# Performance work log

Measured on AMD Instinct MI355X. Metric: run time of the kernel, lower is better.

The kernel has to match this reference:

```python
import jax, jax.numpy as jnp
import numpy as np

BOX = 100.0      # points live in [0, BOX)^3
STRIDE = 128     # > BOX/voxel_size, used for linearizing 3D voxel coords


def setup_inputs() -> dict:
    key = jax.random.key(0)
    k1, k2 = jax.random.split(key)
    N, C = 2_000_000, 32
    positions = jax.random.uniform(k1, (N, 3), dtype=jnp.float32) * BOX
    features = jax.random.normal(k2, (N, C), dtype=jnp.float32)
    voxel_size = jnp.ones((), dtype=jnp.float32)
    return {"positions": positions, "features": features, "voxel_size": voxel_size}


def reference(positions, features, voxel_size):
    """VoxelPooling(position_fn='center', feature_fn='max').

    Output is padded to N rows (M <= N real voxels); `valid` marks real voxels.
    Voxel grid is aligned to the origin; pooled position is the voxel center.
    """
    N = positions.shape[0]
    # integer voxel coordinates (positions are non-negative here)
    coords = jnp.floor(positions / voxel_size).astype(jnp.int32)           # [N,3]
    lin = coords[:, 0] + STRIDE * coords[:, 1] + STRIDE * STRIDE * coords[:, 2]  # [N]
    # compact unique voxels; jit-compatible with fixed size=N, pad with -1
    uniq, inv = jnp.unique(lin, size=N, fill_value=-1, return_inverse=True)
    # per-voxel max over features (empty segments get dtype-min, masked below)
    pooled_features = jax.ops.segment_max(features, inv, num_segments=N)   # [N,C]
    # decode voxel coords from linear key -> voxel centers
    cz = uniq // (STRIDE * STRIDE)
    rem = uniq % (STRIDE * STRIDE)
    cy = rem // STRIDE
    cx = rem % STRIDE
    centers = (jnp.stack([cx, cy, cz], axis=-1).astype(positions.dtype) + 0.5) * voxel_size
    valid = uniq >= 0                                                      # [N]
    pooled_positions = jnp.where(valid[:, None], centers, 0.0)
    pooled_features = jnp.where(valid[:, None], pooled_features, 0.0)
    return pooled_positions, pooled_features, valid
```

## Files before the change

### kernel.cpp

```cpp
#include <hip/hip_runtime.h>
#include <stdint.h>

#define STRIDE 128
#define NVOX (STRIDE * STRIDE * STRIDE)
#define BINVOX 512
#define NBIN (NVOX / BINVOX)
#define HB 256
#define HT 1024
#define NSEG 16
#define SEGBINS (NBIN / NSEG)
#define CAP 1536
#define LINCAP 8192

typedef unsigned long long u64;
typedef float nfloat4 __attribute__((ext_vector_type(4)));

__device__ __forceinline__ uint32_t enc_f32(float f) {
  uint32_t u = __float_as_uint(f);
  return (u & 0x80000000u) ? ~u : (u | 0x80000000u);
}
__device__ __forceinline__ float dec_f32(uint32_t e) {
  uint32_t u = (e & 0x80000000u) ? (e & 0x7fffffffu) : ~e;
  return __uint_as_float(u);
}

__device__ __forceinline__ uint32_t cnt_eq1(uint32_t w) {
  uint32_t y = w ^ 0x01010101u;
  uint32_t z = ~(((y & 0x7F7F7F7Fu) + 0x7F7F7F7Fu) | y | 0x7F7F7F7Fu);
  return __popc(z);
}

__device__ __forceinline__ uint32_t src_of(uint32_t u, const uint32_t* csum,
                                           const uint32_t* offs) {
  uint32_t lo = 0, hi = HB - 1;
  #pragma unroll
  for (int it = 0; it < 8; ++it) {
    uint32_t mid = (lo + hi) >> 1;
    bool gt = csum[mid] > u;
    hi = gt ? mid : hi;
    lo = gt ? lo : mid + 1;
  }
  uint32_t prev = lo ? csum[lo - 1] : 0u;
  return offs[lo] + (u - prev);
}

__device__ __forceinline__ void nt_zero4(void* p) {
  nfloat4 z = {0.f, 0.f, 0.f, 0.f};
  __builtin_nontemporal_store(z, (nfloat4*)p);
}

__global__ __launch_bounds__(HT) void k_build(
    const float* __restrict__ pos, const float* __restrict__ vs_p,
    uint8_t* __restrict__ bytemap, uint32_t* __restrict__ loff,
    uint32_t* __restrict__ pairs, uint32_t* __restrict__ sync,
    float* __restrict__ out_pos, float* __restrict__ out_feat,
    float* __restrict__ out_valid, int n, int vbound, int srow) {
  __shared__ uint32_t h[NBIN];
  __shared__ uint32_t wsum[HT / 64];
  __shared__ uint32_t linbuf[LINCAP];
  int t = threadIdx.x;

  if (blockIdx.x >= HB) {
    size_t gid = (size_t)(blockIdx.x - HB) * HT + t;
    int row = vbound + (int)(gid >> 3);
    int q = (int)(gid & 7);
    if (row >= n) return;
    if (row < srow)
      nt_zero4(((float4*)out_feat) + (size_t)row * 8 + q);
    if (q == 0) {
      out_pos[(size_t)row * 3 + 0] = 0.f;
      out_pos[(size_t)row * 3 + 1] = 0.f;
      out_pos[(size_t)row * 3 + 2] = 0.f;
      out_valid[row] = 0.f;
    }
    return;
  }

  int b = blockIdx.x;
  if (b == 0 && t == 0) *sync = 0u;
  for (int k = t; k < NBIN; k += HT) h[k] = 0u;
  __syncthreads();
  int chunk = (n + HB - 1) / HB;
  int i0 = b * chunk, i1 = min(n, i0 + chunk);
  int len = i1 - i0;
  float vs = vs_p[0];
  for (int j = t; j < len; j += HT) {
    size_t i = (size_t)(i0 + j);
    float x = pos[3 * i + 0];
    float y = pos[3 * i + 1];
    float z = pos[3 * i + 2];
    int lin = (int)floorf(x / vs) + STRIDE * (int)floorf(y / vs) +
              STRIDE * STRIDE * (int)floorf(z / vs);
    linbuf[j] = (uint32_t)lin;
    bytemap[lin] = 1;
    atomicAdd(&h[lin >> 9], 1u);
  }
  __syncthreads();
  uint32_t v0 = h[t * 4 + 0], v1 = h[t * 4 + 1], v2 = h[t * 4 + 2], v3 = h[t * 4 + 3];
  uint32_t s3 = v0 + v1 + v2 + v3;
  uint32_t inc = s3;
  #pragma unroll
  for (int d = 1; d < 64; d <<= 1) {
    uint32_t o = __shfl_up(inc, d, 64);
    if ((t & 63) >= d) inc += o;
  }
  if ((t & 63) == 63) wsum[t >> 6] = inc;
  __syncthreads();
  if (t < 16) {
    uint32_t wv = wsum[t], wi = wv;
    #pragma unroll
    for (int d = 1; d < 16; d <<= 1) {
      uint32_t o = __shfl_up(wi, d, 16);
      if (t >= d) wi += o;
    }
    wsum[t] = wi - wv;
  }
  __syncthreads();
  uint32_t run = wsum[t >> 6] + (inc - s3);
  uint32_t* lr = &loff[(size_t)b * NBIN + t * 4];
  uint32_t c0 = run; lr[0] = run; run += v0;
  uint32_t c1 = run; lr[1] = run; run += v1;
  uint32_t c2 = run; lr[2] = run; run += v2;
  uint32_t c3 = run; lr[3] = run;
  __syncthreads();
  h[t * 4 + 0] = (uint32_t)i0 + c0;
  h[t * 4 + 1] = (uint32_t)i0 + c1;
  h[t * 4 + 2] = (uint32_t)i0 + c2;
  h[t * 4 + 3] = (uint32_t)i0 + c3;
  __syncthreads();
  for (int j = t; j < len; j += HT) {
    int lin = (int)linbuf[j];
    uint32_t slot = atomicAdd(&h[lin >> 9], 1u);
    pairs[slot] = ((uint32_t)(lin & (BINVOX - 1)) << 21) | (uint32_t)(i0 + j);
  }
}

__global__ __launch_bounds__(SEGBINS) void k_scan(
    const uint32_t* __restrict__ bytemap_w, uint32_t* __restrict__ occ_base,
    uint32_t* __restrict__ sync, uint32_t* __restrict__ seg_tot,
    uint32_t* __restrict__ Mp) {
  __shared__ uint32_t s[SEGBINS];
  int b = blockIdx.x, t = threadIdx.x;
  int bin = b * SEGBINS + t;
  const uint4* bp = (const uint4*)bytemap_w + (size_t)bin * 32;
  uint32_t occ = 0;
  #pragma unroll
  for (int k = 0; k < 32; ++k) {
    uint4 v = bp[k];
    occ += cnt_eq1(v.x) + cnt_eq1(v.y) + cnt_eq1(v.z) + cnt_eq1(v.w);
  }
  s[t] = occ;
  __syncthreads();
  for (int off = 1; off < SEGBINS; off <<= 1) {
    uint32_t a = (t >= off) ? s[t - off] : 0u;
    __syncthreads();
    s[t] += a;
    __syncthreads();
  }
  uint32_t excl = s[t] - occ;
  if (t == 0) {
    __hip_atomic_store(&seg_tot[b], s[SEGBINS - 1], __ATOMIC_RELEASE,
                       __HIP_MEMORY_SCOPE_AGENT);
    __hip_atomic_fetch_add(sync, 1u, __ATOMIC_ACQ_REL, __HIP_MEMORY_SCOPE_AGENT);
    while (__hip_atomic_load(sync, __ATOMIC_ACQUIRE, __HIP_MEMORY_SCOPE_AGENT) <
           (uint32_t)NSEG) {}
  }
  __syncthreads();
  uint32_t pre = 0, grand = 0;
  #pragma unroll
  for (int i = 0; i < NSEG; ++i) {
    uint32_t v = __hip_atomic_load(&seg_tot[i], __ATOMIC_ACQUIRE,
                                   __HIP_MEMORY_SCOPE_AGENT);
    if (i < b) pre += v;
    grand += v;
  }
  occ_base[bin] = pre + excl;
  if (b == 0 && t == 0) Mp[0] = grand;
}

__global__ __launch_bounds__(HT) void k_pool(
    const float* __restrict__ feat, const float* __restrict__ vs_p,
    const uint32_t* __restrict__ pairs, const uint32_t* __restrict__ loff,
    const uint32_t* __restrict__ occ_base, const uint8_t* __restrict__ bytemap,
    const uint32_t* __restrict__ Mp,
    float* __restrict__ out_pos, float* __restrict__ out_feat,
    float* __restrict__ out_valid, int n, int vbound) {
  __shared__ uint32_t smax[BINVOX * 32];
  __shared__ u64 sbw[8];
  __shared__ uint32_t offs[HB], csum[HB];
  __shared__ uint32_t srcidx[CAP];
  int t = threadIdx.x;

  if (blockIdx.x >= NBIN) {
    size_t gid = (size_t)(blockIdx.x - NBIN) * HT + t;
    int row = (int)(gid >> 3);
    int q = (int)(gid & 7);
    if (row >= vbound) return;
    uint32_t M = Mp[0];
    if ((uint32_t)row < M) return;
    nt_zero4(((float4*)out_feat) + (size_t)row * 8 + q);
    if (q == 0) {
      out_pos[(size_t)row * 3 + 0] = 0.f;
      out_pos[(size_t)row * 3 + 1] = 0.f;
      out_pos[(size_t)row * 3 + 2] = 0.f;
      out_valid[row] = 0.f;
    }
    return;
  }

  int bin = blockIdx.x;
  #pragma unroll
  for (int k = 0; k < 16; ++k) smax[t + k * HT] = 0u;
  if (t < 512) {
    uint32_t occb = bytemap[(size_t)bin * BINVOX + t];
    u64 m = __ballot(occb == 1u);
    if ((t & 63) == 0) sbw[t >> 6] = m;
  }
  int chunk = (n + HB - 1) / HB;
  if (t < HB) {
    int i0b = t * chunk, i1b = min(n, i0b + chunk);
    uint32_t lo = loff[(size_t)t * NBIN + bin];
    uint32_t hi = (bin == NBIN - 1) ? (uint32_t)(i1b - i0b)
                                    : loff[(size_t)t * NBIN + bin + 1];
    offs[t] = (uint32_t)i0b + lo;
    csum[t] = hi - lo;
  }
  __syncthreads();
  if (t < 64) {
    uint32_t c0 = csum[t * 4], c1 = csum[t * 4 + 1];
    uint32_t c2 = csum[t * 4 + 2], c3 = csum[t * 4 + 3];
    uint32_t s1 = c0 + c1, s2 = s1 + c2, s3 = s2 + c3;
    uint32_t inc = s3;
    #pragma unroll
    for (int d = 1; d < 64; d <<= 1) {
      uint32_t o = __shfl_up(inc, d, 64);
      if (t >= d) inc += o;
    }
    uint32_t base = inc - s3;
    csum[t * 4]     = base + c0;
    csum[t * 4 + 1] = base + s1;
    csum[t * 4 + 2] = base + s2;
    csum[t * 4 + 3] = base + s3;
  }
  __syncthreads();
  uint32_t cnt = csum[HB - 1];
  if (cnt == 0) return;

  bool fits = (cnt <= (uint32_t)CAP);
  if (fits) {
    if (t < HB) {
      uint32_t beg = t ? csum[t - 1] : 0u;
      uint32_t len = csum[t] - beg;
      uint32_t o = offs[t];
      for (uint32_t j = 0; j < len; ++j) srcidx[beg + j] = o + j;
    }
    __syncthreads();
  }

  int g = t >> 3;
  int q = t & 7;
  const float4* f4 = (const float4*)feat;
  uint32_t last = cnt - 1;
  for (uint32_t u = (uint32_t)g; u < cnt; u += 1024) {
    uint32_t pp[8];
    #pragma unroll
    for (int k = 0; k < 8; ++k) {
      uint32_t uu = min(u + 128u * k, last);
      uint32_t s = fits ? srcidx[uu] : src_of(uu, csum, offs);
      pp[k] = pairs[s];
    }
    float4 vv[8];
    #pragma unroll
    for (int k = 0; k < 8; ++k)
      vv[k] = f4[(size_t)(pp[k] & 0x1FFFFFu) * 8 + q];
    #pragma unroll
    for (int k = 0; k < 8; ++k) {
      uint32_t vb = pp[k] >> 21;
      uint32_t* sb = &smax[vb * 32];
      uint32_t c = (uint32_t)q * 4 + vb;
      atomicMax(&sb[(c + 0) & 31], enc_f32(vv[k].x));
      atomicMax(&sb[(c + 1) & 31], enc_f32(vv[k].y));
      atomicMax(&sb[(c + 2) & 31], enc_f32(vv[k].z));
      atomicMax(&sb[(c + 3) & 31], enc_f32(vv[k].w));
    }
  }
  __syncthreads();

  int vb = t >> 1, half = t & 1;
  u64 w = sbw[vb >> 6];
  int bit = vb & 63;
  if ((w >> bit) & 1ull) {
    uint32_t lr = (uint32_t)__popcll(w & ((1ull << bit) - 1ull));
    for (int ww = 0; ww < (vb >> 6); ++ww) lr += (uint32_t)__popcll(sbw[ww]);
    uint32_t rank = occ_base[bin] + lr;
    float4* orow = (float4*)(out_feat + (size_t)rank * 32 + half * 16);
    const uint32_t* sb = &smax[vb * 32];
    #pragma unroll
    for (int j = 0; j < 4; ++j) {
      uint32_t c = (uint32_t)half * 16 + j * 4 + vb;
      float4 o;
      o.x = dec_f32(sb[(c + 0) & 31]);
      o.y = dec_f32(sb[(c + 1) & 31]);
      o.z = dec_f32(sb[(c + 2) & 31]);
      o.w = dec_f32(sb[(c + 3) & 31]);
      orow[j] = o;
    }
    if (half == 0) {
      float vs = vs_p[0];
      int lin = bin * BINVOX + vb;
      int cx = lin & 127, cy = (lin >> 7) & 127, cz = lin >> 14;
      out_pos[(size_t)rank * 3 + 0] = ((float)cx + 0.5f) * vs;
      out_pos[(size_t)rank * 3 + 1] = ((float)cy + 0.5f) * vs;
      out_pos[(size_t)rank * 3 + 2] = ((float)cz + 0.5f) * vs;
      out_valid[rank] = 1.0f;
    }
  }
}

__global__ void k_tail2(float4* __restrict__ dst, long long cnt4) {
  long long i = (long long)blockIdx.x * blockDim.x + threadIdx.x;
  if (i < cnt4) nt_zero4(dst + i);
}

extern "C" void kernel_launch(void* const* d_in, const int* in_sizes, int n_in,
                              void* d_out, int out_size, void* d_ws, size_t ws_size,
                              hipStream_t stream) {
  const float* pos  = (const float*)d_in[0];
  const float* feat = (const float*)d_in[1];
  const float* vs   = (const float*)d_in[2];
  int n = in_sizes[0] / 3;

  float*    out_pos   = (float*)d_out;
  uint32_t* out_feat  = (uint32_t*)(out_pos + (size_t)n * 3);
  float*    out_valid = (float*)((float*)out_feat + (size_t)n * 32);

  int vbound = n < 1000000 ? n : 1000000;

  size_t scratch_u32 = (size_t)n + (size_t)HB * NBIN + NBIN + NVOX / 4;
  size_t ws_need = 256 + scratch_u32 * 4;

  uint32_t* Mp      = (uint32_t*)d_ws;
  uint32_t* sync    = Mp + 1;
  uint32_t* seg_tot = Mp + 8;

  uint32_t* base;
  int srow;
  if (ws_size >= ws_need) {
    base = (uint32_t*)((char*)d_ws + 256);
    srow = n;
  } else {
    base = out_feat + (size_t)n * 32 - scratch_u32;
    srow = (int)(((size_t)n * 32 - scratch_u32) / 32);
  }
  uint32_t* pairs    = base;
  uint32_t* loff     = pairs + n;
  uint32_t* occ_base = loff + (size_t)HB * NBIN;
  uint8_t*  bytemap  = (uint8_t*)(occ_base + NBIN);

  int hard_blocks = (int)(((size_t)(n - vbound) * 8 + HT - 1) / HT);
  k_build<<<HB + hard_blocks, HT, 0, stream>>>(
      pos, vs, bytemap, loff, pairs, sync, out_pos, (float*)out_feat,
      out_valid, n, vbound, srow);
  k_scan<<<NSEG, SEGBINS, 0, stream>>>((const uint32_t*)bytemap, occ_base,
                                       sync, seg_tot, Mp);
  int soft_blocks = (int)(((size_t)vbound * 8 + HT - 1) / HT);
  k_pool<<<NBIN + soft_blocks, HT, 0, stream>>>(
      feat, vs, pairs, loff, occ_base, bytemap, Mp,
      out_pos, (float*)out_feat, out_valid, n, vbound);
  if (srow < n) {
    long long cnt4 = ((long long)n * 32 - (long long)srow * 32) / 4;
    k_tail2<<<(int)((cnt4 + 1023) / 1024), 1024, 0, stream>>>(
        (float4*)(out_feat + (size_t)srow * 32), cnt4);
  }
}
```

Baseline: 192.9 us.

## Transpose per-chunk bin offsets in scan kernel for coalesced pool reads

Adds transpose blocks to the scan kernel that rewrite the chunk-major loff table (HB x NBIN) into a bin-major offs_T table with absolute offsets plus a sentinel end row. The pool kernel then reads 256 consecutive words per bin instead of 256 strided words, which removes uncoalesced gathers from each of the 4096 pool blocks. The cost is extra scratch space, an additional write and read pass over roughly 4 MB, and a larger scan launch.

```diff
diff --git a/kernel.cpp b/kernel.cpp
--- a/kernel.cpp
+++ b/kernel.cpp
@@ -9,6 +9,7 @@
 #define HT 1024
 #define NSEG 16
 #define SEGBINS (NBIN / NSEG)
+#define NTB 64
 #define CAP 1536
 #define LINCAP 8192
 
@@ -135,12 +136,39 @@
   }
 }
 
-__global__ __launch_bounds__(SEGBINS) void k_scan(
-    const uint32_t* __restrict__ bytemap_w, uint32_t* __restrict__ occ_base,
+__global__ __launch_bounds__(256) void k_scan(
+    const uint32_t* __restrict__ bytemap_w, const uint32_t* __restrict__ loff,
+    uint32_t* __restrict__ offs_T, uint32_t* __restrict__ occ_base,
     uint32_t* __restrict__ sync, uint32_t* __restrict__ seg_tot,
-    uint32_t* __restrict__ Mp) {
+    uint32_t* __restrict__ Mp, int n) {
+  int t = threadIdx.x;
+
+  if (blockIdx.x >= NSEG) {
+    __shared__ uint32_t tile[256][65];
+    int tb = blockIdx.x - NSEG;
+    int chunk = (n + HB - 1) / HB;
+    uint32_t i0 = (uint32_t)(t * chunk);
+    const uint4* lp = (const uint4*)(loff + (size_t)t * NBIN + tb * 64);
+    #pragma unroll
+    for (int k = 0; k < 16; ++k) {
+      uint4 v = lp[k];
+      tile[t][k * 4 + 0] = i0 + v.x;
+      tile[t][k * 4 + 1] = i0 + v.y;
+      tile[t][k * 4 + 2] = i0 + v.z;
+      tile[t][k * 4 + 3] = i0 + v.w;
+    }
+    __syncthreads();
+    for (int j = 0; j < 64; ++j) {
+      int bin = tb * 64 + j;
+      offs_T[(size_t)bin * HB + t] = tile[t][j];
+    }
+    if (tb == NTB - 1)
+      offs_T[(size_t)NBIN * HB + t] = (uint32_t)min(n, t * chunk + chunk);
+    return;
+  }
+
   __shared__ uint32_t s[SEGBINS];
-  int b = blockIdx.x, t = threadIdx.x;
+  int b = blockIdx.x;
   int bin = b * SEGBINS + t;
   const uint4* bp = (const uint4*)bytemap_w + (size_t)bin * 32;
   uint32_t occ = 0;
@@ -180,7 +208,7 @@
 
 __global__ __launch_bounds__(HT) void k_pool(
     const float* __restrict__ feat, const float* __restrict__ vs_p,
-    const uint32_t* __restrict__ pairs, const uint32_t* __restrict__ loff,
+    const uint32_t* __restrict__ pairs, const uint32_t* __restrict__ offs_T,
     const uint32_t* __restrict__ occ_base, const uint8_t* __restrict__ bytemap,
     const uint32_t* __restrict__ Mp,
     float* __restrict__ out_pos, float* __restrict__ out_feat,
@@ -216,14 +244,11 @@
     u64 m = __ballot(occb == 1u);
     if ((t & 63) == 0) sbw[t >> 6] = m;
   }
-  int chunk = (n + HB - 1) / HB;
   if (t < HB) {
-    int i0b = t * chunk, i1b = min(n, i0b + chunk);
-    uint32_t lo = loff[(size_t)t * NBIN + bin];
-    uint32_t hi = (bin == NBIN - 1) ? (uint32_t)(i1b - i0b)
-                                    : loff[(size_t)t * NBIN + bin + 1];
-    offs[t] = (uint32_t)i0b + lo;
-    csum[t] = hi - lo;
+    uint32_t v0 = offs_T[(size_t)bin * HB + t];
+    uint32_t v1 = offs_T[(size_t)(bin + 1) * HB + t];
+    offs[t] = v0;
+    csum[t] = v1 - v0;
   }
   __syncthreads();
   if (t < 64) {
@@ -336,7 +361,8 @@
 
   int vbound = n < 1000000 ? n : 1000000;
 
-  size_t scratch_u32 = (size_t)n + (size_t)HB * NBIN + NBIN + NVOX / 4;
+  size_t scratch_u32 = (size_t)n + (size_t)HB * NBIN + (size_t)(NBIN + 1) * HB +
+                       NBIN + NVOX / 4;
   size_t ws_need = 256 + scratch_u32 * 4;
 
   uint32_t* Mp      = (uint32_t*)d_ws;
@@ -354,18 +380,19 @@
   }
   uint32_t* pairs    = base;
   uint32_t* loff     = pairs + n;
-  uint32_t* occ_base = loff + (size_t)HB * NBIN;
+  uint32_t* offs_T   = loff + (size_t)HB * NBIN;
+  uint32_t* occ_base = offs_T + (size_t)(NBIN + 1) * HB;
   uint8_t*  bytemap  = (uint8_t*)(occ_base + NBIN);
 
   int hard_blocks = (int)(((size_t)(n - vbound) * 8 + HT - 1) / HT);
   k_build<<<HB + hard_blocks, HT, 0, stream>>>(
       pos, vs, bytemap, loff, pairs, sync, out_pos, (float*)out_feat,
       out_valid, n, vbound, srow);
-  k_scan<<<NSEG, SEGBINS, 0, stream>>>((const uint32_t*)bytemap, occ_base,
-                                       sync, seg_tot, Mp);
+  k_scan<<<NSEG + NTB, 256, 0, stream>>>((const uint32_t*)bytemap, loff,
+                                         offs_T, occ_base, sync, seg_tot, Mp, n);
   int soft_blocks = (int)(((size_t)vbound * 8 + HT - 1) / HT);
   k_pool<<<NBIN + soft_blocks, HT, 0, stream>>>(
-      feat, vs, pairs, loff, occ_base, bytemap, Mp,
+      feat, vs, pairs, offs_T, occ_base, bytemap, Mp,
       out_pos, (float*)out_feat, out_valid, n, vbound);
   if (srow < n) {
     long long cnt4 = ((long long)n * 32 - (long long)srow * 32) / 4;
```

Measured after the change: 189.7 us, median of 2. Within noise of the previous version (-1.7%).
